# Kernel optimization log

Hardware: AMD Instinct MI355X
Metric: run time of the kernel (lower is better)

## Reference

```python
import jax, jax.numpy as jnp
import numpy as np

B, S, D, HU = 64, 512, 256, 1024
W_SCALE = 0.01  # flax nn.initializers.normal() default stddev


def setup_inputs() -> dict:
    key = jax.random.key(0)
    ks = jax.random.split(key, 13)
    inp = {
        "inputs": jax.random.normal(ks[0], (B, S, D), dtype=jnp.float32),
        "H0": jax.random.normal(ks[1], (B, HU), dtype=jnp.float32),
        "C0": jax.random.normal(ks[2], (B, HU), dtype=jnp.float32),
        "Wxi": jax.random.normal(ks[3], (D, HU), dtype=jnp.float32) * W_SCALE,
        "Whi": jax.random.normal(ks[4], (HU, HU), dtype=jnp.float32) * W_SCALE,
        "bi": jnp.zeros((HU,), dtype=jnp.float32),
        "Wxf": jax.random.normal(ks[5], (D, HU), dtype=jnp.float32) * W_SCALE,
        "Whf": jax.random.normal(ks[6], (HU, HU), dtype=jnp.float32) * W_SCALE,
        "bf": jnp.zeros((HU,), dtype=jnp.float32),
        "Wxo": jax.random.normal(ks[7], (D, HU), dtype=jnp.float32) * W_SCALE,
        "Who": jax.random.normal(ks[8], (HU, HU), dtype=jnp.float32) * W_SCALE,
        "bo": jnp.zeros((HU,), dtype=jnp.float32),
        "Wxc": jax.random.normal(ks[9], (D, HU), dtype=jnp.float32) * W_SCALE,
        "Whc": jax.random.normal(ks[10], (HU, HU), dtype=jnp.float32) * W_SCALE,
        "bc": jnp.zeros((HU,), dtype=jnp.float32),
        "Wd": jax.random.normal(ks[11], (HU, 1), dtype=jnp.float32) * W_SCALE,
        "bd": jnp.zeros((1,), dtype=jnp.float32),
    }
    return inp


def _lstm_forward(inputs, H0, C0, Wxi, Whi, bi, Wxf, Whf, bf,
                  Wxo, Who, bo, Wxc, Whc, bc, Wd, bd):
    Hn = H0.shape[1]
    # Pack the 4 gate projections so the input GEMM is done once for all timesteps.
    Wx = jnp.concatenate([Wxi, Wxf, Wxo, Wxc], axis=1)  # (D, 4H)
    Wh = jnp.concatenate([Whi, Whf, Who, Whc], axis=1)  # (H, 4H)
    b = jnp.concatenate([bi, bf, bo, bc])                # (4H,)
    xg = jnp.einsum('bsd,dk->bsk', inputs, Wx) + b       # (B, S, 4H)

    def step(carry, xg_t):
        H, C = carry
        g = xg_t + H @ Wh                                # (B, 4H)
        i = jax.nn.sigmoid(g[:, :Hn])
        f = jax.nn.sigmoid(g[:, Hn:2 * Hn])
        o = jax.nn.sigmoid(g[:, 2 * Hn:3 * Hn])
        c_tilde = jnp.tanh(g[:, 3 * Hn:])
        C = f * C + i * c_tilde
        H = o * jnp.tanh(C)
        return (H, C), H

    (Hf, Cf), Hs = jax.lax.scan(step, (H0, C0), jnp.swapaxes(xg, 0, 1))
    outputs = jnp.swapaxes(Hs, 0, 1)                     # (B, S, H)
    pred = outputs @ Wd + bd                             # (B, S, 1)
    return pred, (Hf, Cf)


def reference(inputs, H0, C0, Wxi, Whi, bi, Wxf, Whf, bf,
              Wxo, Who, bo, Wxc, Whc, bc, Wd, bd):
    return _lstm_forward(inputs, H0, C0, Wxi, Whi, bi, Wxf, Whf, bf,
                         Wxo, Who, bo, Wxc, Whc, bc, Wd, bd)
```

## Files before the change

### kernel.cpp

```cpp
#include <hip/hip_runtime.h>


#define NB   128
#define SEQ  512
#define BATCH 64
#define DIM  256
#define HU   1024
#define ROWU 1032

typedef unsigned short u16;
typedef unsigned int   u32;
typedef unsigned long long u64;
typedef __attribute__((ext_vector_type(8))) short  short8;
typedef __attribute__((ext_vector_type(4))) float  f32x4;

typedef const __attribute__((address_space(1))) void* gptr_t;
typedef __attribute__((address_space(3))) void*       lptr_t;

__device__ __forceinline__ u16 f2bf(float x) {
  u32 u = __float_as_uint(x);
  u32 r = (u + 0x7FFFu + ((u >> 16) & 1u)) >> 16;
  return (u16)r;
}
__device__ __forceinline__ float sigf(float x)  { return 1.0f / (1.0f + __expf(-x)); }
__device__ __forceinline__ float tanhfast(float x) { return 1.0f - 2.0f / (1.0f + __expf(2.0f * x)); }
__device__ __forceinline__ short8 cv8(uint4 v) {
  union { uint4 d; short8 s; } u; u.d = v; return u.s;
}


__global__ void k_prep(const float* __restrict__ H0, u16* __restrict__ Hbuf0,
                       u32* __restrict__ flags) {
  int i = blockIdx.x * 256 + threadIdx.x;
  if (i < 2048) flags[i] = 0u;
  Hbuf0[i] = f2bf(H0[i]);
}

__global__ void k_xconv(const float* __restrict__ in, u16* __restrict__ out) {
  int i = blockIdx.x * 256 + threadIdx.x;
  float4 v = ((const float4*)in)[i];
  ushort4 o;
  o.x = f2bf(v.x); o.y = f2bf(v.y); o.z = f2bf(v.z); o.w = f2bf(v.w);
  ((ushort4*)out)[i] = o;
}

__global__ void k_pack(const float* __restrict__ Wxi, const float* __restrict__ Whi,
                       const float* __restrict__ Wxf, const float* __restrict__ Whf,
                       const float* __restrict__ Wxo, const float* __restrict__ Who,
                       const float* __restrict__ Wxc, const float* __restrict__ Whc,
                       u16* __restrict__ Wpack) {
  int tid  = blockIdx.x * 256 + threadIdx.x;
  int lane = tid & 63;
  int kc   = (tid >> 6) % 40;
  int nt   = ((tid >> 6) / 40) & 7;
  int bj   = (tid >> 6) / 320;
  int c    = nt * 16 + (lane & 15);
  int gate = (c >> 3) & 3;
  int h    = bj * 32 + (c >> 5) * 8 + (c & 7);
  const float* Wx = (gate == 0) ? Wxi : (gate == 1) ? Wxf : (gate == 2) ? Wxo : Wxc;
  const float* Wh = (gate == 0) ? Whi : (gate == 1) ? Whf : (gate == 2) ? Who : Whc;
  int kbase = kc * 32 + ((lane >> 4) << 3);
  u16 tmp[8];
#pragma unroll
  for (int e = 0; e < 8; e++) {
    int k = kbase + e;
    float v = (k < DIM) ? Wx[k * HU + h] : Wh[(k - DIM) * HU + h];
    tmp[e] = f2bf(v);
  }
  *(uint4*)(Wpack + (size_t)tid * 8) = *(uint4*)tmp;
}

__global__ void k_predsum(const float* __restrict__ part, const float* __restrict__ bd,
                          float* __restrict__ pred) {
  int i = blockIdx.x * 256 + threadIdx.x;
  int b = i & 63, t = i >> 6;
  float s = bd[0];
  const float* p0 = part + (size_t)t * NB * 64 + b;
#pragma unroll 8
  for (int jj = 0; jj < NB; jj++) s += p0[jj * 64];
  pred[b * SEQ + t] = s;
}


struct MainParams {
  const u16* __restrict__ xbf;
  const u16* __restrict__ Wpack;
  u16* __restrict__ Hbuf;
  const float* __restrict__ C0;
  const float* __restrict__ Wd;
  const float* __restrict__ bi;
  const float* __restrict__ bfg;
  const float* __restrict__ bo;
  const float* __restrict__ bc;
  float* __restrict__ ppart;
  float* __restrict__ Hf;
  float* __restrict__ Cf;
  u32* __restrict__ flags;
};

__global__ __launch_bounds__(256, 1) void lstm_main(MainParams p) {
  __shared__ __align__(16) u16 Hsm[16 * ROWU];

  const int tid  = threadIdx.x;
  const int wv   = tid >> 6, lane = tid & 63;
  const int bj   = blockIdx.x >> 2, bb = blockIdx.x & 3;
  const int q    = lane >> 4;
  const int q8   = q * 8;
  const int m16  = lane & 15;
  const int hl   = lane & 7;
  const bool hiH = (lane & 8) != 0;

  const int hglob = bj * 32 + wv * 8 + hl;
  const int row0  = 16 * bb;

  short8 wx[8][2], wh[32][2];
  {
    const u16* wbase = p.Wpack + ((size_t)bj * 8 + 2 * wv) * (40 * 512) + lane * 8;
#pragma unroll
    for (int kc = 0; kc < 8; kc++)
#pragma unroll
      for (int ntl = 0; ntl < 2; ntl++)
        wx[kc][ntl] = *(const short8*)(wbase + ((size_t)ntl * 40 + kc) * 512);
#pragma unroll
    for (int kc = 0; kc < 32; kc++)
#pragma unroll
      for (int ntl = 0; ntl < 2; ntl++)
        wh[kc][ntl] = *(const short8*)(wbase + ((size_t)ntl * 40 + 8 + kc) * 512);
  }

  const float bI = p.bi[hglob],  bF = p.bfg[hglob];
  const float bO = p.bo[hglob],  bC = p.bc[hglob];
  const float wdv = p.Wd[hglob];
  float Cst[4], Hst[4];
#pragma unroll
  for (int r = 0; r < 4; r++) {
    Cst[r] = p.C0[(row0 + q * 4 + r) * HU + hglob];
    Hst[r] = 0.f;
  }

  const u16* Aw = Hsm + m16 * ROWU + q8;

  uint4 ax[8];
#pragma unroll
  for (int kc = 0; kc < 8; kc++)
    ax[kc] = *(const uint4*)(p.xbf + ((size_t)((row0 + m16) * SEQ + 0)) * DIM
                             + kc * 32 + q8);

#pragma unroll 1
  for (int t = 0; t < SEQ; t++) {
    const int rb = t & 1;
    const u16* Hr = p.Hbuf + (size_t)rb * (BATCH * HU);
    u16*       Hw = p.Hbuf + (size_t)(rb ^ 1) * (BATCH * HU);

#pragma unroll
    for (int i = 0; i < 8; i++) {
      int s = wv * 8 + i, row = s >> 1, half = s & 1;
      const u16* g = Hr + (size_t)(row0 + row) * HU + half * 512 + lane * 8;
      __builtin_amdgcn_global_load_lds((gptr_t)(const void*)g,
          (lptr_t)(void*)(Hsm + row * ROWU + half * 512), 16, 0, 17);
    }

    f32x4 acc[2][4];
#pragma unroll
    for (int ntl = 0; ntl < 2; ntl++)
#pragma unroll
      for (int c = 0; c < 4; c++) acc[ntl][c] = (f32x4){0.f, 0.f, 0.f, 0.f};
#pragma unroll
    for (int kc = 0; kc < 8; kc++) {
      short8 af = cv8(ax[kc]);
      acc[0][kc & 3] = __builtin_amdgcn_mfma_f32_16x16x32_bf16(af, wx[kc][0], acc[0][kc & 3], 0, 0, 0);
      acc[1][kc & 3] = __builtin_amdgcn_mfma_f32_16x16x32_bf16(af, wx[kc][1], acc[1][kc & 3], 0, 0, 0);
    }

    __syncthreads();

    {
      const int tn = (t + 1 < SEQ) ? t + 1 : t;
#pragma unroll
      for (int kc = 0; kc < 8; kc++)
        ax[kc] = *(const uint4*)(p.xbf + ((size_t)((row0 + m16) * SEQ + tn)) * DIM
                                 + kc * 32 + q8);
    }

#pragma unroll
    for (int kc = 0; kc < 32; kc++) {
      short8 af = *(const short8*)(Aw + kc * 32);
      acc[0][kc & 3] = __builtin_amdgcn_mfma_f32_16x16x32_bf16(af, wh[kc][0], acc[0][kc & 3], 0, 0, 0);
      acc[1][kc & 3] = __builtin_amdgcn_mfma_f32_16x16x32_bf16(af, wh[kc][1], acc[1][kc & 3], 0, 0, 0);
    }

    f32x4 g01 = (acc[0][0] + acc[0][1]) + (acc[0][2] + acc[0][3]);
    f32x4 g23 = (acc[1][0] + acc[1][1]) + (acc[1][2] + acc[1][3]);

    float pr[4];
#pragma unroll
    for (int r = 0; r < 4; r++) {
      float u0 = g01[r], u1 = g23[r];
      float v0 = __shfl_xor(u0, 8);
      float v1 = __shfl_xor(u1, 8);
      float gi = hiH ? v0 : u0, gf = hiH ? u0 : v0;
      float go = hiH ? v1 : u1, gc = hiH ? u1 : v1;
      float iv = sigf(gi + bI), fv = sigf(gf + bF);
      float ov = sigf(go + bO), ct = tanhfast(gc + bC);
      Cst[r] = fv * Cst[r] + iv * ct;
      Hst[r] = ov * tanhfast(Cst[r]);
      pr[r]  = Hst[r] * wdv;
    }

    if (!hiH) {
#pragma unroll
      for (int r = 0; r < 4; r++)
        __hip_atomic_store(Hw + (size_t)(row0 + q * 4 + r) * HU + hglob,
                           f2bf(Hst[r]), __ATOMIC_RELAXED, __HIP_MEMORY_SCOPE_AGENT);
    }

#pragma unroll
    for (int r = 0; r < 4; r++) {
      pr[r] += __shfl_xor(pr[r], 1);
      pr[r] += __shfl_xor(pr[r], 2);
      pr[r] += __shfl_xor(pr[r], 4);
    }
    if (m16 == 0) {
      float4 st = {pr[0], pr[1], pr[2], pr[3]};
      *(float4*)(p.ppart + (((size_t)t * 32 + bj) * 4 + wv) * 64 + row0 + q * 4) = st;
    }

    __syncthreads();
    if (tid == 0)
      __hip_atomic_store(p.flags + (bb * 32 + bj) * 16, (u32)(t + 1),
                         __ATOMIC_RELAXED, __HIP_MEMORY_SCOPE_AGENT);
    if (tid < 32) {
      const u32* f = p.flags + (bb * 32 + tid) * 16;
      while (__hip_atomic_load(f, __ATOMIC_RELAXED, __HIP_MEMORY_SCOPE_AGENT) < (u32)(t + 1))
        __builtin_amdgcn_s_sleep(1);
    }
    __syncthreads();
  }

  if (!hiH) {
#pragma unroll
    for (int r = 0; r < 4; r++) {
      int row = row0 + q * 4 + r;
      p.Hf[row * HU + hglob] = Hst[r];
      p.Cf[row * HU + hglob] = Cst[r];
    }
  }
}


extern "C" void kernel_launch(void* const* d_in, const int* in_sizes, int n_in,
                              void* d_out, int out_size, void* d_ws, size_t ws_size,
                              hipStream_t stream) {
  const float* inputs = (const float*)d_in[0];
  const float* H0  = (const float*)d_in[1];
  const float* C0  = (const float*)d_in[2];
  const float* Wxi = (const float*)d_in[3];
  const float* Whi = (const float*)d_in[4];
  const float* bi  = (const float*)d_in[5];
  const float* Wxf = (const float*)d_in[6];
  const float* Whf = (const float*)d_in[7];
  const float* bf_ = (const float*)d_in[8];
  const float* Wxo = (const float*)d_in[9];
  const float* Who = (const float*)d_in[10];
  const float* bo  = (const float*)d_in[11];
  const float* Wxc = (const float*)d_in[12];
  const float* Whc = (const float*)d_in[13];
  const float* bc  = (const float*)d_in[14];
  const float* Wd  = (const float*)d_in[15];
  const float* bd  = (const float*)d_in[16];

  char* ws = (char*)d_ws;
  u32*   flags = (u32*)ws;
  u16*   Wpack = (u16*)(ws + 8192);
  u16*   xbf   = (u16*)(ws + 8192 + 10485760);
  u16*   Hbuf  = (u16*)(ws + 8192 + 10485760 + 16777216);
  float* ppart = (float*)(ws + 8192 + 10485760 + 16777216 + 262144);

  float* pred = (float*)d_out;
  float* Hf   = pred + BATCH * SEQ;
  float* Cf   = Hf + BATCH * HU;

  k_prep<<<256, 256, 0, stream>>>(H0, Hbuf, flags);
  k_xconv<<<8192, 256, 0, stream>>>(inputs, xbf);
  k_pack<<<2560, 256, 0, stream>>>(Wxi, Whi, Wxf, Whf, Wxo, Who, Wxc, Whc, Wpack);

  MainParams prm{xbf, Wpack, Hbuf, C0, Wd, bi, bf_, bo, bc, ppart, Hf, Cf, flags};
  lstm_main<<<dim3(NB), dim3(256), 0, stream>>>(prm);

  k_predsum<<<128, 256, 0, stream>>>(ppart, bd, pred);
}
```

Measured before the change: 2.341 ms.

## Pin LSTM batch groups to single XCDs and sync via local L2

The kernel now launches 256 blocks, reads each block's XCC id, and runs a cross-block handshake. If every XCD holds exactly 32 blocks, the blocks on XCDs 0-3 each take one batch slice, so all blocks that exchange H for that slice share one L2. The per-step H exchange and step flags then use workgroup-scope stores, sc0 loads and a non-bypassing cache policy, replacing device-scope coherent traffic. The prefetch of the next x timestep is moved after the barrier, and the trailing __syncthreads is removed. This relies on undocumented placement and coherence behaviour, with a fallback to the old agent-scope path when the mapping check fails.

```diff
diff --git a/kernel.cpp b/kernel.cpp
--- a/kernel.cpp
+++ b/kernel.cpp
@@ -1,12 +1,22 @@
 #include <hip/hip_runtime.h>
 
 
-#define NB   128
-#define SEQ  512
+#define NB    128
+#define GRID  256
+#define SEQ   512
 #define BATCH 64
-#define DIM  256
-#define HU   1024
-#define ROWU 1032
+#define DIM   256
+#define HU    1024
+#define ROWU  1032
+
+#define F_STEP 0
+#define F_XMAP 512
+#define F_TOK  768
+#define F_DEC1 1024
+#define F_DEC2 1025
+#define F_VER  1026
+
+#define HWREG_XCC_ID_IMM ((31 << 11) | 20)
 
 typedef unsigned short u16;
 typedef unsigned int   u32;
@@ -27,12 +37,30 @@
 __device__ __forceinline__ short8 cv8(uint4 v) {
   union { uint4 d; short8 s; } u; u.d = v; return u.s;
 }
+__device__ __forceinline__ u32 l2_load(const u32* p) {
+  u64 a = (u64)p; u32 v;
+  asm volatile("global_load_dword %0, %1, off sc0\n\ts_waitcnt vmcnt(0)"
+               : "=v"(v) : "v"(a) : "memory");
+  return v;
+}
+__device__ __forceinline__ void st_wg_u32(u32* p, u32 v) {
+  __hip_atomic_store(p, v, __ATOMIC_RELAXED, __HIP_MEMORY_SCOPE_WORKGROUP);
+}
+__device__ __forceinline__ void st_wg_u16(u16* p, u16 v) {
+  __hip_atomic_store(p, v, __ATOMIC_RELAXED, __HIP_MEMORY_SCOPE_WORKGROUP);
+}
+__device__ __forceinline__ u32 ld_ag(const u32* p) {
+  return __hip_atomic_load(p, __ATOMIC_RELAXED, __HIP_MEMORY_SCOPE_AGENT);
+}
+__device__ __forceinline__ void st_ag_u32(u32* p, u32 v) {
+  __hip_atomic_store(p, v, __ATOMIC_RELAXED, __HIP_MEMORY_SCOPE_AGENT);
+}
 
 
 __global__ void k_prep(const float* __restrict__ H0, u16* __restrict__ Hbuf0,
                        u32* __restrict__ flags) {
   int i = blockIdx.x * 256 + threadIdx.x;
-  if (i < 2048) flags[i] = 0u;
+  if (i < 4096) flags[i] = 0u;
   Hbuf0[i] = f2bf(H0[i]);
 }
 
@@ -100,10 +128,132 @@
 
 __global__ __launch_bounds__(256, 1) void lstm_main(MainParams p) {
   __shared__ __align__(16) u16 Hsm[16 * ROWU];
+  __shared__ int s_roles[4];
 
   const int tid  = threadIdx.x;
   const int wv   = tid >> 6, lane = tid & 63;
-  const int bj   = blockIdx.x >> 2, bb = blockIdx.x & 3;
+  const int bid  = blockIdx.x;
+
+  u32* xmap = p.flags + F_XMAP;
+  u32* tok  = p.flags + F_TOK;
+  u32* d1   = p.flags + F_DEC1;
+  u32* d2   = p.flags + F_DEC2;
+  u32* ver  = p.flags + F_VER;
+
+  const u32 myxcc = ((u32)__builtin_amdgcn_s_getreg(HWREG_XCC_ID_IMM)) & 7u;
+
+  if (tid == 0) st_ag_u32(xmap + bid, 0x100u | myxcc);
+
+  u32* smap = (u32*)Hsm;
+  {
+    u32 v = 0; int spins = 0;
+    for (;;) {
+      v = ld_ag(xmap + tid);
+      if (v & 0x100u) break;
+      if (ld_ag(d1) != 0u) break;
+      if (++spins > 20000) break;
+      __builtin_amdgcn_s_sleep(2);
+    }
+    smap[tid] = v;
+  }
+  __syncthreads();
+  if (tid == 0) {
+    int cnt[8] = {0, 0, 0, 0, 0, 0, 0, 0};
+    bool all = true;
+    for (int i = 0; i < 256; i++) {
+      u32 v = smap[i];
+      if (!(v & 0x100u)) { all = false; break; }
+      cnt[v & 7u]++;
+    }
+    bool ok = all;
+    if (ok)
+      for (int x = 0; x < 8; x++) ok = ok && (cnt[x] == 32);
+    u32 want = ok ? 2u : 1u, exp = 0u, dec = want;
+    if (!__hip_atomic_compare_exchange_strong(d1, &exp, want,
+          __ATOMIC_RELAXED, __ATOMIC_RELAXED, __HIP_MEMORY_SCOPE_AGENT))
+      dec = exp;
+    s_roles[3] = (int)dec;
+    s_roles[2] = 0;
+  }
+  __syncthreads();
+  int dec = s_roles[3];
+  int myrank = 0;
+
+  if (dec == 2) {
+    {
+      u32 v = smap[tid];
+      if (!(v & 0x100u)) {
+        int spins = 0;
+        do {
+          v = ld_ag(xmap + tid);
+          if (++spins > 100000) break;
+        } while (!(v & 0x100u));
+        smap[tid] = v;
+      }
+    }
+    __syncthreads();
+    if (tid == 0) {
+      bool okh = true;
+      for (int i = 0; i < 256; i++) okh = okh && ((smap[i] & 0x100u) != 0u);
+      int rank = 0;
+      if (okh) {
+        for (int i = 0; i < bid; i++) rank += ((smap[i] & 7u) == myxcc) ? 1 : 0;
+        st_wg_u32(tok + myxcc * 32 + rank, 1u);
+        int spins = 0;
+        for (;;) {
+          bool allt = true;
+          for (int j = 0; j < 32; j++)
+            allt = allt && (l2_load(tok + myxcc * 32 + j) != 0u);
+          if (allt) break;
+          if (ld_ag(d2) != 0u) { okh = false; break; }
+          if (++spins > 20000) { okh = false; break; }
+          __builtin_amdgcn_s_sleep(1);
+        }
+      }
+      u32 got;
+      if (okh) {
+        __hip_atomic_fetch_add(ver, 1u, __ATOMIC_RELAXED, __HIP_MEMORY_SCOPE_AGENT);
+        int spins = 0;
+        for (;;) {
+          u32 dv = ld_ag(d2);
+          if (dv != 0u) { got = dv; break; }
+          if (ld_ag(ver) >= 256u) {
+            u32 exp = 0u; got = 2u;
+            if (!__hip_atomic_compare_exchange_strong(d2, &exp, 2u,
+                  __ATOMIC_RELAXED, __ATOMIC_RELAXED, __HIP_MEMORY_SCOPE_AGENT))
+              got = exp;
+            break;
+          }
+          if (++spins > 100000) {
+            u32 exp = 0u; got = 1u;
+            if (!__hip_atomic_compare_exchange_strong(d2, &exp, 1u,
+                  __ATOMIC_RELAXED, __ATOMIC_RELAXED, __HIP_MEMORY_SCOPE_AGENT))
+              got = exp;
+            break;
+          }
+          __builtin_amdgcn_s_sleep(1);
+        }
+      } else {
+        u32 exp = 0u; got = 1u;
+        if (!__hip_atomic_compare_exchange_strong(d2, &exp, 1u,
+              __ATOMIC_RELAXED, __ATOMIC_RELAXED, __HIP_MEMORY_SCOPE_AGENT))
+          got = exp;
+      }
+      s_roles[3] = (int)got;
+      s_roles[2] = rank;
+    }
+    __syncthreads();
+    dec    = s_roles[3];
+    myrank = s_roles[2];
+  }
+
+  const bool fast = (dec == 2);
+  int workf, bb, bj;
+  if (fast) { workf = (myxcc < 4u) ? 1 : 0; bb = (int)myxcc; bj = myrank; }
+  else      { workf = (bid < NB) ? 1 : 0;   bb = bid & 3;    bj = bid >> 2; }
+  if (!workf) return;
+  __syncthreads();
+
   const int q    = lane >> 4;
   const int q8   = q * 8;
   const int m16  = lane & 15;
@@ -152,12 +302,22 @@
     const u16* Hr = p.Hbuf + (size_t)rb * (BATCH * HU);
     u16*       Hw = p.Hbuf + (size_t)(rb ^ 1) * (BATCH * HU);
 
-#pragma unroll
-    for (int i = 0; i < 8; i++) {
-      int s = wv * 8 + i, row = s >> 1, half = s & 1;
-      const u16* g = Hr + (size_t)(row0 + row) * HU + half * 512 + lane * 8;
-      __builtin_amdgcn_global_load_lds((gptr_t)(const void*)g,
-          (lptr_t)(void*)(Hsm + row * ROWU + half * 512), 16, 0, 17);
+    if (fast) {
+#pragma unroll
+      for (int i = 0; i < 8; i++) {
+        int s = wv * 8 + i, row = s >> 1, half = s & 1;
+        const u16* g = Hr + (size_t)(row0 + row) * HU + half * 512 + lane * 8;
+        __builtin_amdgcn_global_load_lds((gptr_t)(const void*)g,
+            (lptr_t)(void*)(Hsm + row * ROWU + half * 512), 16, 0, 1);
+      }
+    } else {
+#pragma unroll
+      for (int i = 0; i < 8; i++) {
+        int s = wv * 8 + i, row = s >> 1, half = s & 1;
+        const u16* g = Hr + (size_t)(row0 + row) * HU + half * 512 + lane * 8;
+        __builtin_amdgcn_global_load_lds((gptr_t)(const void*)g,
+            (lptr_t)(void*)(Hsm + row * ROWU + half * 512), 16, 0, 17);
+      }
     }
 
     f32x4 acc[2][4];
@@ -173,14 +333,6 @@
     }
 
     __syncthreads();
-
-    {
-      const int tn = (t + 1 < SEQ) ? t + 1 : t;
-#pragma unroll
-      for (int kc = 0; kc < 8; kc++)
-        ax[kc] = *(const uint4*)(p.xbf + ((size_t)((row0 + m16) * SEQ + tn)) * DIM
-                                 + kc * 32 + q8);
-    }
 
 #pragma unroll
     for (int kc = 0; kc < 32; kc++) {
@@ -208,10 +360,16 @@
     }
 
     if (!hiH) {
-#pragma unroll
-      for (int r = 0; r < 4; r++)
-        __hip_atomic_store(Hw + (size_t)(row0 + q * 4 + r) * HU + hglob,
-                           f2bf(Hst[r]), __ATOMIC_RELAXED, __HIP_MEMORY_SCOPE_AGENT);
+      if (fast) {
+#pragma unroll
+        for (int r = 0; r < 4; r++)
+          st_wg_u16(Hw + (size_t)(row0 + q * 4 + r) * HU + hglob, f2bf(Hst[r]));
+      } else {
+#pragma unroll
+        for (int r = 0; r < 4; r++)
+          __hip_atomic_store(Hw + (size_t)(row0 + q * 4 + r) * HU + hglob,
+                             f2bf(Hst[r]), __ATOMIC_RELAXED, __HIP_MEMORY_SCOPE_AGENT);
+      }
     }
 
 #pragma unroll
@@ -226,15 +384,28 @@
     }
 
     __syncthreads();
-    if (tid == 0)
-      __hip_atomic_store(p.flags + (bb * 32 + bj) * 16, (u32)(t + 1),
-                         __ATOMIC_RELAXED, __HIP_MEMORY_SCOPE_AGENT);
-    if (tid < 32) {
-      const u32* f = p.flags + (bb * 32 + tid) * 16;
-      while (__hip_atomic_load(f, __ATOMIC_RELAXED, __HIP_MEMORY_SCOPE_AGENT) < (u32)(t + 1))
-        __builtin_amdgcn_s_sleep(1);
-    }
-    __syncthreads();
+
+    {
+      const int tn = (t + 1 < SEQ) ? t + 1 : t;
+#pragma unroll
+      for (int kc = 0; kc < 8; kc++)
+        ax[kc] = *(const uint4*)(p.xbf + ((size_t)((row0 + m16) * SEQ + tn)) * DIM
+                                 + kc * 32 + q8);
+    }
+
+    const u32 tf = (u32)(t + 1);
+    if (tid == 0) {
+      if (fast) st_wg_u32(p.flags + F_STEP + bb * 32 + bj, tf);
+      else      st_ag_u32(p.flags + F_STEP + bb * 32 + bj, tf);
+    }
+    if (lane < 32) {
+      const u32* fp = p.flags + F_STEP + bb * 32 + lane;
+      if (fast) {
+        while (l2_load(fp) < tf) __builtin_amdgcn_s_sleep(1);
+      } else {
+        while (ld_ag(fp) < tf) __builtin_amdgcn_s_sleep(1);
+      }
+    }
   }
 
   if (!hiH) {
@@ -271,10 +442,10 @@
 
   char* ws = (char*)d_ws;
   u32*   flags = (u32*)ws;
-  u16*   Wpack = (u16*)(ws + 8192);
-  u16*   xbf   = (u16*)(ws + 8192 + 10485760);
-  u16*   Hbuf  = (u16*)(ws + 8192 + 10485760 + 16777216);
-  float* ppart = (float*)(ws + 8192 + 10485760 + 16777216 + 262144);
+  u16*   Wpack = (u16*)(ws + 16384);
+  u16*   xbf   = (u16*)(ws + 16384 + 10485760);
+  u16*   Hbuf  = (u16*)(ws + 16384 + 10485760 + 16777216);
+  float* ppart = (float*)(ws + 16384 + 10485760 + 16777216 + 262144);
 
   float* pred = (float*)d_out;
   float* Hf   = pred + BATCH * SEQ;
@@ -285,7 +456,7 @@
   k_pack<<<2560, 256, 0, stream>>>(Wxi, Whi, Wxf, Whf, Wxo, Who, Wxc, Whc, Wpack);
 
   MainParams prm{xbf, Wpack, Hbuf, C0, Wd, bi, bf_, bo, bc, ppart, Hf, Cf, flags};
-  lstm_main<<<dim3(NB), dim3(256), 0, stream>>>(prm);
+  lstm_main<<<dim3(GRID), dim3(256), 0, stream>>>(prm);
 
   k_predsum<<<128, 256, 0, stream>>>(ppart, bd, pred);
 }
```

New measurement: 7.998 ms. +241.7%, slower.

## Map batch groups to single XCDs to use XCD-local L2 synchronization

Applied to the files above, without the earlier changes.

Launches twice as many blocks, reads each block's XCD id from a hardware register, and runs a two-phase consensus protocol. If every XCD holds exactly 32 blocks, each batch group of 32 blocks is assigned to one XCD and the extra blocks exit. On this fast path the per-step flag exchange and H broadcast use workgroup-scope stores and L2-level loads instead of device-scope coherence, so cross-block sync stays inside one XCD's L2 and should be cheaper. The cost is a more complex startup handshake with timeouts and a fallback to the original mapping. Correctness depends on assumptions about cache coherence within an XCD.

```diff
diff --git a/kernel.cpp b/kernel.cpp
--- a/kernel.cpp
+++ b/kernel.cpp
@@ -1,12 +1,23 @@
 #include <hip/hip_runtime.h>
 
 
-#define NB   128
-#define SEQ  512
+#define NB    128
+#define GRID  256
+#define SEQ   512
 #define BATCH 64
-#define DIM  256
-#define HU   1024
-#define ROWU 1032
+#define DIM   256
+#define HU    1024
+#define ROWU  1032
+
+#define F_STEP 0
+#define F_XMAP 2048
+#define F_TOK  2304
+#define F_CNT  2560
+#define F_DEC1 2561
+#define F_DEC2 2562
+#define F_VER  2563
+
+#define HWREG_XCC_ID_IMM ((31 << 11) | 20)
 
 typedef unsigned short u16;
 typedef unsigned int   u32;
@@ -27,12 +38,37 @@
 __device__ __forceinline__ short8 cv8(uint4 v) {
   union { uint4 d; short8 s; } u; u.d = v; return u.s;
 }
+__device__ __forceinline__ u32 l2_load(const u32* p) {
+  u64 a = (u64)p; u32 v;
+  asm volatile("global_load_dword %0, %1, off sc0\n\ts_waitcnt vmcnt(0)"
+               : "=v"(v) : "v"(a) : "memory");
+  return v;
+}
+__device__ __forceinline__ void st_wg_u32(u32* p, u32 v) {
+  __hip_atomic_store(p, v, __ATOMIC_RELAXED, __HIP_MEMORY_SCOPE_WORKGROUP);
+}
+__device__ __forceinline__ void st_wg_u16(u16* p, u16 v) {
+  __hip_atomic_store(p, v, __ATOMIC_RELAXED, __HIP_MEMORY_SCOPE_WORKGROUP);
+}
+__device__ __forceinline__ u32 ld_ag(const u32* p) {
+  return __hip_atomic_load(p, __ATOMIC_RELAXED, __HIP_MEMORY_SCOPE_AGENT);
+}
+__device__ __forceinline__ void st_ag_u32(u32* p, u32 v) {
+  __hip_atomic_store(p, v, __ATOMIC_RELAXED, __HIP_MEMORY_SCOPE_AGENT);
+}
+__device__ __forceinline__ u32 cas_dec(u32* p, u32 want) {
+  u32 exp = 0u;
+  if (__hip_atomic_compare_exchange_strong(p, &exp, want,
+        __ATOMIC_RELEASE, __ATOMIC_ACQUIRE, __HIP_MEMORY_SCOPE_AGENT))
+    return want;
+  return exp;
+}
 
 
 __global__ void k_prep(const float* __restrict__ H0, u16* __restrict__ Hbuf0,
                        u32* __restrict__ flags) {
   int i = blockIdx.x * 256 + threadIdx.x;
-  if (i < 2048) flags[i] = 0u;
+  if (i < 4096) flags[i] = 0u;
   Hbuf0[i] = f2bf(H0[i]);
 }
 
@@ -100,10 +136,107 @@
 
 __global__ __launch_bounds__(256, 1) void lstm_main(MainParams p) {
   __shared__ __align__(16) u16 Hsm[16 * ROWU];
+  __shared__ int s_rank, s_dec;
 
   const int tid  = threadIdx.x;
   const int wv   = tid >> 6, lane = tid & 63;
-  const int bj   = blockIdx.x >> 2, bb = blockIdx.x & 3;
+  const int bid  = blockIdx.x;
+
+  u32* xmap = p.flags + F_XMAP;
+  u32* tok  = p.flags + F_TOK;
+  u32* cnt  = p.flags + F_CNT;
+  u32* d1   = p.flags + F_DEC1;
+  u32* d2   = p.flags + F_DEC2;
+  u32* ver  = p.flags + F_VER;
+
+  const u32 myxcc = ((u32)__builtin_amdgcn_s_getreg(HWREG_XCC_ID_IMM)) & 7u;
+
+  if (tid == 0) {
+    st_ag_u32(xmap + bid, 0x100u | myxcc);
+    __hip_atomic_fetch_add(cnt, 1u, __ATOMIC_RELEASE, __HIP_MEMORY_SCOPE_AGENT);
+
+    u32 dec1;
+    if (bid == 0) {
+      bool ok = false; int sp = 0;
+      while (sp++ < 2500) {
+        if (__hip_atomic_load(cnt, __ATOMIC_ACQUIRE, __HIP_MEMORY_SCOPE_AGENT) >= (u32)GRID)
+          { ok = true; break; }
+        __builtin_amdgcn_s_sleep(1);
+      }
+      if (ok) {
+        int c8[8] = {0,0,0,0,0,0,0,0};
+        for (int i = 0; i < GRID; i++) {
+          u32 v = ld_ag(xmap + i);
+          if (!(v & 0x100u)) { ok = false; break; }
+          c8[v & 7u]++;
+        }
+        if (ok)
+          for (int x = 0; x < 8; x++) ok = ok && (c8[x] == 32);
+      }
+      dec1 = cas_dec(d1, ok ? 2u : 1u);
+    } else {
+      int sp = 0;
+      for (;;) {
+        dec1 = __hip_atomic_load(d1, __ATOMIC_ACQUIRE, __HIP_MEMORY_SCOPE_AGENT);
+        if (dec1 != 0u) break;
+        if (sp++ > 6000) { dec1 = cas_dec(d1, 1u); break; }
+        __builtin_amdgcn_s_sleep(1);
+      }
+    }
+
+    int rank = 0;
+    u32 dec2 = 1u;
+    if (dec1 == 2u) {
+      for (int i = 0; i < bid; i++)
+        rank += ((ld_ag(xmap + i) & 7u) == myxcc) ? 1 : 0;
+      st_wg_u32(tok + (int)myxcc * 32 + rank, 1u);
+      bool okh = false; int sp = 0;
+      for (;;) {
+        bool all = true;
+        for (int j = 0; j < 32; j++)
+          all = all && (l2_load(tok + (int)myxcc * 32 + j) != 0u);
+        if (all) { okh = true; break; }
+        if (ld_ag(d2) != 0u) break;
+        if (sp++ > 200) break;
+        __builtin_amdgcn_s_sleep(1);
+      }
+      if (okh)
+        __hip_atomic_fetch_add(ver, 1u, __ATOMIC_RELEASE, __HIP_MEMORY_SCOPE_AGENT);
+      else
+        (void)cas_dec(d2, 1u);
+
+      if (bid == 0) {
+        int sp2 = 0;
+        for (;;) {
+          u32 dv = ld_ag(d2);
+          if (dv != 0u) { dec2 = dv; break; }
+          if (__hip_atomic_load(ver, __ATOMIC_ACQUIRE, __HIP_MEMORY_SCOPE_AGENT) >= (u32)GRID)
+            { dec2 = cas_dec(d2, 2u); break; }
+          if (sp2++ > 3000) { dec2 = cas_dec(d2, 1u); break; }
+          __builtin_amdgcn_s_sleep(1);
+        }
+      } else {
+        int sp2 = 0;
+        for (;;) {
+          u32 dv = ld_ag(d2);
+          if (dv != 0u) { dec2 = dv; break; }
+          if (sp2++ > 6000) { dec2 = cas_dec(d2, 1u); break; }
+          __builtin_amdgcn_s_sleep(1);
+        }
+      }
+    }
+    s_rank = rank;
+    s_dec  = (dec1 == 2u) ? (int)dec2 : 1;
+  }
+  __syncthreads();
+  const bool fast  = (s_dec == 2);
+  const int myrank = s_rank;
+
+  int workf, bb, bj;
+  if (fast) { workf = (myxcc < 4u) ? 1 : 0; bb = (int)myxcc; bj = myrank; }
+  else      { workf = (bid < NB) ? 1 : 0;   bb = bid & 3;    bj = bid >> 2; }
+  if (!workf) return;
+
   const int q    = lane >> 4;
   const int q8   = q * 8;
   const int m16  = lane & 15;
@@ -156,8 +289,12 @@
     for (int i = 0; i < 8; i++) {
       int s = wv * 8 + i, row = s >> 1, half = s & 1;
       const u16* g = Hr + (size_t)(row0 + row) * HU + half * 512 + lane * 8;
-      __builtin_amdgcn_global_load_lds((gptr_t)(const void*)g,
-          (lptr_t)(void*)(Hsm + row * ROWU + half * 512), 16, 0, 17);
+      if (fast)
+        __builtin_amdgcn_global_load_lds((gptr_t)(const void*)g,
+            (lptr_t)(void*)(Hsm + row * ROWU + half * 512), 16, 0, 1);
+      else
+        __builtin_amdgcn_global_load_lds((gptr_t)(const void*)g,
+            (lptr_t)(void*)(Hsm + row * ROWU + half * 512), 16, 0, 17);
     }
 
     f32x4 acc[2][4];
@@ -208,10 +345,16 @@
     }
 
     if (!hiH) {
-#pragma unroll
-      for (int r = 0; r < 4; r++)
-        __hip_atomic_store(Hw + (size_t)(row0 + q * 4 + r) * HU + hglob,
-                           f2bf(Hst[r]), __ATOMIC_RELAXED, __HIP_MEMORY_SCOPE_AGENT);
+      if (fast) {
+#pragma unroll
+        for (int r = 0; r < 4; r++)
+          st_wg_u16(Hw + (size_t)(row0 + q * 4 + r) * HU + hglob, f2bf(Hst[r]));
+      } else {
+#pragma unroll
+        for (int r = 0; r < 4; r++)
+          __hip_atomic_store(Hw + (size_t)(row0 + q * 4 + r) * HU + hglob,
+                             f2bf(Hst[r]), __ATOMIC_RELAXED, __HIP_MEMORY_SCOPE_AGENT);
+      }
     }
 
 #pragma unroll
@@ -226,13 +369,15 @@
     }
 
     __syncthreads();
-    if (tid == 0)
-      __hip_atomic_store(p.flags + (bb * 32 + bj) * 16, (u32)(t + 1),
-                         __ATOMIC_RELAXED, __HIP_MEMORY_SCOPE_AGENT);
+    const u32 tf = (u32)(t + 1);
+    if (tid == 0) {
+      if (fast) st_wg_u32(p.flags + F_STEP + (bb * 32 + bj) * 16, tf);
+      else      st_ag_u32(p.flags + F_STEP + (bb * 32 + bj) * 16, tf);
+    }
     if (tid < 32) {
-      const u32* f = p.flags + (bb * 32 + tid) * 16;
-      while (__hip_atomic_load(f, __ATOMIC_RELAXED, __HIP_MEMORY_SCOPE_AGENT) < (u32)(t + 1))
-        __builtin_amdgcn_s_sleep(1);
+      const u32* fp = p.flags + F_STEP + (bb * 32 + tid) * 16;
+      if (fast) { while (l2_load(fp) < tf) __builtin_amdgcn_s_sleep(1); }
+      else      { while (ld_ag(fp)  < tf) __builtin_amdgcn_s_sleep(1); }
     }
     __syncthreads();
   }
@@ -271,10 +416,10 @@
 
   char* ws = (char*)d_ws;
   u32*   flags = (u32*)ws;
-  u16*   Wpack = (u16*)(ws + 8192);
-  u16*   xbf   = (u16*)(ws + 8192 + 10485760);
-  u16*   Hbuf  = (u16*)(ws + 8192 + 10485760 + 16777216);
-  float* ppart = (float*)(ws + 8192 + 10485760 + 16777216 + 262144);
+  u16*   Wpack = (u16*)(ws + 16384);
+  u16*   xbf   = (u16*)(ws + 16384 + 10485760);
+  u16*   Hbuf  = (u16*)(ws + 16384 + 10485760 + 16777216);
+  float* ppart = (float*)(ws + 16384 + 10485760 + 16777216 + 262144);
 
   float* pred = (float*)d_out;
   float* Hf   = pred + BATCH * SEQ;
@@ -285,7 +430,7 @@
   k_pack<<<2560, 256, 0, stream>>>(Wxi, Whi, Wxf, Whf, Wxo, Who, Wxc, Whc, Wpack);
 
   MainParams prm{xbf, Wpack, Hbuf, C0, Wd, bi, bf_, bo, bc, ppart, Hf, Cf, flags};
-  lstm_main<<<dim3(NB), dim3(256), 0, stream>>>(prm);
+  lstm_main<<<dim3(GRID), dim3(256), 0, stream>>>(prm);
 
   k_predsum<<<128, 256, 0, stream>>>(ppart, bd, pred);
 }
```

New measurement: 2.703 ms. 1.15x slower.
